# Kernel tuning notes

Hardware: AMD Instinct MI355X
Metric: run time of the kernel (lower is better)

Reference implementation:

```python
import jax, jax.numpy as jnp
import numpy as np

N_NODES = 50000
N_EDGES = 600000
D_IN = 128
D_OUT = 128

def setup_inputs() -> dict:
    key = jax.random.key(0)
    k1, k2, k3, k4 = jax.random.split(key, 4)
    x = jax.random.normal(k1, (N_NODES, D_IN), dtype=jnp.float32)
    edge_index = jax.random.randint(k2, (2, N_EDGES), 0, N_NODES, dtype=jnp.int64)
    # Linear weights stored as (in, out) so y = x @ W + b; scaled like torch default init
    W1 = jax.random.normal(k3, (2 * D_IN, D_OUT), dtype=jnp.float32) * (1.0 / np.sqrt(2 * D_IN))
    b1 = jnp.zeros((D_OUT,), dtype=jnp.float32)
    W2 = jax.random.normal(k4, (D_OUT, D_OUT), dtype=jnp.float32) * (1.0 / np.sqrt(D_OUT))
    b2 = jnp.zeros((D_OUT,), dtype=jnp.float32)
    return {"x": x, "edge_index": edge_index, "W1": W1, "b1": b1, "W2": W2, "b2": b2}

def reference(x, edge_index, W1, b1, W2, b2):
    row, col = edge_index[0], edge_index[1]
    x_col = x[col]                       # [E, D_IN]
    feat = jnp.concatenate([x_col, x[row] - x_col], axis=-1)  # [E, 2*D_IN]
    h = jax.nn.relu(feat @ W1 + b1)      # [E, D_OUT]
    messages = h @ W2 + b2               # [E, D_OUT]
    # max aggregation into nodes, empty segments -> -inf -> 0
    out = jax.ops.segment_max(messages, col, num_segments=x.shape[0])
    out = jnp.where(jnp.isneginf(out), jnp.zeros_like(out), out)
    return out
```

## Files before the change

### kernel.cpp

```cpp
#include <hip/hip_runtime.h>

typedef __attribute__((ext_vector_type(8))) _Float16 f16x8;
typedef __attribute__((ext_vector_type(4))) _Float16 f16x4;
typedef __attribute__((ext_vector_type(4))) float f32x4;

#define D 128
#define NCH 256
#define BNODES 16
#define TILE 64
#define SC_ILP 4
#define PSTRIDE 136

static __device__ __forceinline__ ushort f2h(float f) {
    _Float16 h = (_Float16)f;
    return __builtin_bit_cast(ushort, h);
}

__global__ void prep_kernel(const float* __restrict__ W1,
                            const float* __restrict__ W2,
                            const int* __restrict__ ecol,
                            ushort* __restrict__ w1abt,
                            ushort* __restrict__ w2t,
                            int* __restrict__ hist,
                            int* __restrict__ rank,
                            int E, int n_nodes)
{
    int gid = blockIdx.x * blockDim.x + threadIdx.x;
    if (gid < NCH * D) {
        int oc = gid >> 7, k = gid & 127;
        float v;
        if (oc < 128) v = W1[k * D + oc] - W1[(k + 128) * D + oc];
        else          v = W1[(k + 128) * D + (oc - 128)];
        w1abt[gid] = f2h(v);
    } else if (gid < NCH * D + D * D) {
        int id2 = gid - NCH * D;
        int oc = id2 >> 7, k = id2 & 127;
        w2t[id2] = f2h(W2[k * D + oc]);
    } else {
        int e = gid - (NCH * D + D * D);
        if (e < E) {
            int c = ecol[e];
            if ((unsigned)c >= (unsigned)n_nodes) c = 0;
            rank[e] = atomicAdd(&hist[c], 1);
        }
    }
}

__global__ void scan1_kernel(const int* __restrict__ hist, int* __restrict__ partial, int N)
{
    __shared__ int s[256];
    int tid = threadIdx.x;
    int i = blockIdx.x * 256 + tid;
    s[tid] = (i < N) ? hist[i] : 0;
    __syncthreads();
    #pragma unroll
    for (int off = 128; off > 0; off >>= 1) {
        if (tid < off) s[tid] += s[tid + off];
        __syncthreads();
    }
    if (tid == 0) partial[blockIdx.x] = s[0];
}

__global__ void scan23_kernel(const int* __restrict__ hist, const int* __restrict__ partial,
                              int* __restrict__ ofs,
                              int nb, int N, int E)
{
    __shared__ int sp[256];
    __shared__ int s[256];
    int tid = threadIdx.x;

    int pv = (tid < nb) ? partial[tid] : 0;
    sp[tid] = pv;
    __syncthreads();
    #pragma unroll
    for (int off = 1; off < 256; off <<= 1) {
        int t = (tid >= off) ? sp[tid - off] : 0;
        __syncthreads();
        sp[tid] += t;
        __syncthreads();
    }
    const int bofs = (blockIdx.x > 0) ? sp[blockIdx.x - 1] : 0;

    int i = blockIdx.x * 256 + tid;
    int v = (i < N) ? hist[i] : 0;
    s[tid] = v;
    __syncthreads();
    #pragma unroll
    for (int off = 1; off < 256; off <<= 1) {
        int t = (tid >= off) ? s[tid - off] : 0;
        __syncthreads();
        s[tid] += t;
        __syncthreads();
    }
    if (i < N) ofs[i] = bofs + s[tid] - v;
    if (blockIdx.x == 0 && tid == 0) ofs[N] = E;
}

__global__ __launch_bounds__(256) void scatter_pab_kernel(
    const float* __restrict__ x,
    const ushort* __restrict__ w1abt,
    const float* __restrict__ b1,
    ushort* __restrict__ pab,
    const int* __restrict__ erow, const int* __restrict__ ecol,
    const int* __restrict__ nofs,
    const int* __restrict__ rank,
    unsigned* __restrict__ spk,
    int E, int n_nodes, int npab)
{
    __shared__ ushort A[64 * 128];
    const int tid = threadIdx.x;

    if ((int)blockIdx.x >= npab) {
        const int stride = (gridDim.x - npab) * 256;
        const int e0 = ((int)blockIdx.x - npab) * 256 + tid;
        int cc[SC_ILP], rr[SC_ILP], rk[SC_ILP];
        #pragma unroll
        for (int j = 0; j < SC_ILP; ++j) {
            int e = e0 + j * stride;
            if (e < E) {
                int c = ecol[e];
                if ((unsigned)c >= (unsigned)n_nodes) c = 0;
                int r = erow[e];
                if ((unsigned)r >= (unsigned)n_nodes) r = 0;
                cc[j] = c; rr[j] = r; rk[j] = rank[e];
            } else cc[j] = -1;
        }
        int pos[SC_ILP];
        #pragma unroll
        for (int j = 0; j < SC_ILP; ++j)
            if (cc[j] >= 0) pos[j] = nofs[cc[j]] + rk[j];
        #pragma unroll
        for (int j = 0; j < SC_ILP; ++j)
            if (cc[j] >= 0) spk[pos[j]] = (unsigned)cc[j] | ((unsigned)rr[j] << 16);
        return;
    }

    const int base = blockIdx.x * 64;

    #pragma unroll
    for (int it = 0; it < 8; ++it) {
        int idx4 = it * 256 + tid;
        int row = idx4 >> 5;
        int c4  = idx4 & 31;
        int node = base + row;
        float4 vx = make_float4(0.f, 0.f, 0.f, 0.f);
        if (node < n_nodes) vx = ((const float4*)x)[(size_t)node * 32 + c4];
        f16x4 o;
        o[0] = (_Float16)vx.x; o[1] = (_Float16)vx.y;
        o[2] = (_Float16)vx.z; o[3] = (_Float16)vx.w;
        *(f16x4*)((char*)A + row * 256 + ((c4 * 8) ^ ((row & 7) << 4))) = o;
    }
    __syncthreads();

    const int l = tid & 63, w = tid >> 6;
    const int l15 = l & 15, lq = l >> 4;

    f32x4 acc[4][4];
    #pragma unroll
    for (int cf = 0; cf < 4; ++cf)
        #pragma unroll
        for (int rf = 0; rf < 4; ++rf)
            acc[cf][rf] = (f32x4){0.f, 0.f, 0.f, 0.f};

    #pragma unroll
    for (int kk = 0; kk < 4; ++kk) {
        f16x8 a[4], b[4];
        #pragma unroll
        for (int cf = 0; cf < 4; ++cf)
            a[cf] = *(const f16x8*)(w1abt + (w * 64 + cf * 16 + l15) * 128 + kk * 32 + lq * 8);
        #pragma unroll
        for (int rf = 0; rf < 4; ++rf) {
            int row = rf * 16 + l15;
            b[rf] = *(const f16x8*)((const char*)A + row * 256 + ((kk * 64 + lq * 16) ^ ((row & 7) << 4)));
        }
        #pragma unroll
        for (int cf = 0; cf < 4; ++cf)
            #pragma unroll
            for (int rf = 0; rf < 4; ++rf)
                acc[cf][rf] = __builtin_amdgcn_mfma_f32_16x16x32_f16(a[cf], b[rf], acc[cf][rf], 0, 0, 0);
    }

    #pragma unroll
    for (int rf = 0; rf < 4; ++rf) {
        int node = base + rf * 16 + l15;
        if (node < n_nodes) {
            #pragma unroll
            for (int cf = 0; cf < 4; ++cf) {
                int ch = w * 64 + cf * 16 + lq * 4;
                float4 bb = (w < 2) ? *(const float4*)(b1 + ch) : make_float4(0.f, 0.f, 0.f, 0.f);
                f16x4 o;
                o[0] = (_Float16)(acc[cf][rf][0] + bb.x);
                o[1] = (_Float16)(acc[cf][rf][1] + bb.y);
                o[2] = (_Float16)(acc[cf][rf][2] + bb.z);
                o[3] = (_Float16)(acc[cf][rf][3] + bb.w);
                *(f16x4*)(pab + (size_t)node * NCH + ch) = o;
            }
        }
    }
}

__global__ __launch_bounds__(256, 4) void edgeconv_main(
    const ushort* __restrict__ pab,
    const ushort* __restrict__ w2t,
    const unsigned* __restrict__ spk,
    const int* __restrict__ nofs,
    const float* __restrict__ b2,
    float* __restrict__ out,
    int E, int n_nodes)
{
    __shared__ unsigned outbuf[BNODES * D];
    __shared__ ushort Hs[TILE * D];
    __shared__ ushort PaL[BNODES * PSTRIDE];
    __shared__ int colidx[TILE];
    __shared__ int rowidx[TILE];

    const int tid = threadIdx.x;

    const int nwg = gridDim.x, orig = blockIdx.x;
    const int q = nwg >> 3, rr = nwg & 7, xcd = orig & 7;
    const int bucket = (xcd < rr ? xcd * (q + 1) : rr * (q + 1) + (xcd - rr) * q) + (orig >> 3);

    const int base = bucket * BNODES;
    const int nend = min(base + BNODES, n_nodes);
    const int estart = nofs[base];
    const int eend = nofs[nend];

    #pragma unroll
    for (int i = 0; i < 8; ++i) outbuf[tid + i * 256] = 0u;

    const int l = tid & 63, w = tid >> 6;
    const int l15 = l & 15, lq = l >> 4;
    const int cg = tid & 15, esub = tid >> 4;
    const f16x8 zero = {0, 0, 0, 0, 0, 0, 0, 0};
    const unsigned padp = (unsigned)base | ((unsigned)base << 16);

    {
        int node = tid >> 4;
        int ch = (tid & 15) * 8;
        int gn = base + node;
        f16x8 v = zero;
        if (gn < n_nodes) v = *(const f16x8*)(pab + (size_t)gn * NCH + ch);
        *(f16x8*)(PaL + node * PSTRIDE + ch) = v;
    }

    unsigned px = padp;
    if (tid < TILE && estart + tid < eend) px = spk[estart + tid];

    for (int t0 = estart; t0 < eend; t0 += TILE) {
        const int n = min(TILE, eend - t0);
        __syncthreads();
        if (tid < TILE) {
            colidx[tid] = (int)(px & 0xffffu);
            rowidx[tid] = (int)(px >> 16);
            int nt = t0 + TILE + tid;
            px = (nt < eend) ? spk[nt] : padp;
        }
        __syncthreads();

        {
            f16x8 vb[4];
            #pragma unroll
            for (int it = 0; it < 4; ++it) {
                int e = it * 16 + esub;
                int r = rowidx[e];
                vb[it] = *(const f16x8*)(pab + (size_t)r * NCH + 128 + cg * 8);
            }
            #pragma unroll
            for (int it = 0; it < 4; ++it) {
                int e = it * 16 + esub;
                int c = colidx[e] - base;
                f16x8 va = *(const f16x8*)(PaL + c * PSTRIDE + cg * 8);
                f16x8 h = __builtin_elementwise_max(va + vb[it], zero);
                *(f16x8*)((char*)Hs + e * 256 + ((cg * 16) ^ ((e & 7) << 4))) = h;
            }
        }
        __syncthreads();

        f32x4 acc[4][2];
        #pragma unroll
        for (int mf = 0; mf < 4; ++mf)
            #pragma unroll
            for (int nf = 0; nf < 2; ++nf)
                acc[mf][nf] = (f32x4){0.f, 0.f, 0.f, 0.f};

        #pragma unroll
        for (int kk = 0; kk < 4; ++kk) {
            f16x8 a[4], b[2];
            #pragma unroll
            for (int mf = 0; mf < 4; ++mf) {
                int row = mf * 16 + l15;
                a[mf] = *(const f16x8*)((const char*)Hs + row * 256 + ((kk * 64 + lq * 16) ^ ((row & 7) << 4)));
            }
            #pragma unroll
            for (int nf = 0; nf < 2; ++nf) {
                int col = w * 32 + nf * 16 + l15;
                b[nf] = *(const f16x8*)(w2t + col * 128 + kk * 32 + lq * 8);
            }
            #pragma unroll
            for (int mf = 0; mf < 4; ++mf)
                #pragma unroll
                for (int nf = 0; nf < 2; ++nf)
                    acc[mf][nf] = __builtin_amdgcn_mfma_f32_16x16x32_f16(a[mf], b[nf], acc[mf][nf], 0, 0, 0);
        }

        #pragma unroll
        for (int nf = 0; nf < 2; ++nf) {
            int col = w * 32 + nf * 16 + l15;
            #pragma unroll
            for (int mf = 0; mf < 4; ++mf) {
                #pragma unroll
                for (int r = 0; r < 4; ++r) {
                    int row = mf * 16 + lq * 4 + r;
                    if (row < n) {
                        int node = colidx[row] - base;
                        unsigned bs = __float_as_uint(acc[mf][nf][r]);
                        unsigned enc = (bs & 0x80000000u) ? ~bs : (bs | 0x80000000u);
                        atomicMax(&outbuf[node * D + col], enc);
                    }
                }
            }
        }
    }
    __syncthreads();

    const int n0 = tid >> 4;
    const int c0 = (tid & 15) * 8;
    const int gnode = base + n0;
    if (gnode < n_nodes) {
        #pragma unroll
        for (int j = 0; j < 2; ++j) {
            float4 o;
            #pragma unroll
            for (int k = 0; k < 4; ++k) {
                int ch = c0 + j * 4 + k;
                unsigned u = outbuf[n0 * D + ch];
                float v;
                if (u == 0u) v = 0.f;
                else {
                    unsigned bs = (u & 0x80000000u) ? (u & 0x7fffffffu) : ~u;
                    v = __uint_as_float(bs) + b2[ch];
                }
                ((float*)&o)[k] = v;
            }
            *(float4*)(out + (size_t)gnode * D + c0 + j * 4) = o;
        }
    }
}

extern "C" void kernel_launch(void* const* d_in, const int* in_sizes, int n_in,
                              void* d_out, int out_size, void* d_ws, size_t ws_size,
                              hipStream_t stream)
{
    const float* x  = (const float*)d_in[0];
    const int* eidx = (const int*)d_in[1];
    const float* W1 = (const float*)d_in[2];
    const float* b1 = (const float*)d_in[3];
    const float* W2 = (const float*)d_in[4];
    const float* b2 = (const float*)d_in[5];

    const int n_nodes = in_sizes[0] / D;
    const int E = in_sizes[1] / 2;
    const int* erow = eidx;
    const int* ecol = eidx + E;

    const int nb_scan = (n_nodes + 255) / 256;
    const int nbuckets = (n_nodes + BNODES - 1) / BNODES;
    const int npab = (n_nodes + 63) / 64;
    const int nsc = (E + 256 * SC_ILP - 1) / (256 * SC_ILP);

    char* ws = (char*)d_ws;
    size_t off = 0;
    ushort* pab = (ushort*)(ws + off);   off += (size_t)n_nodes * NCH * sizeof(ushort);
    off = (off + 255) & ~(size_t)255;
    ushort* w1abt = (ushort*)(ws + off); off += (size_t)NCH * D * sizeof(ushort);
    ushort* w2t = (ushort*)(ws + off);   off += (size_t)D * D * sizeof(ushort);
    off = (off + 255) & ~(size_t)255;
    int* hist = (int*)(ws + off);        off += (size_t)n_nodes * 4;
    off = (off + 255) & ~(size_t)255;
    int* nofs = (int*)(ws + off);        off += (size_t)(n_nodes + 1) * 4;
    off = (off + 255) & ~(size_t)255;
    int* rank = (int*)(ws + off);        off += (size_t)E * 4;
    off = (off + 255) & ~(size_t)255;
    int* partial = (int*)(ws + off);     off += 256 * 4;
    off = (off + 255) & ~(size_t)255;
    unsigned* spk = (unsigned*)(ws + off); off += (size_t)E * 4;

    float* out = (float*)d_out;

    hipMemsetAsync(hist, 0, (size_t)n_nodes * sizeof(int), stream);

    const int prep_work = NCH * D + D * D + E;
    prep_kernel<<<(prep_work + 255) / 256, 256, 0, stream>>>(W1, W2, ecol, w1abt, w2t, hist, rank, E, n_nodes);

    scan1_kernel<<<nb_scan, 256, 0, stream>>>(hist, partial, n_nodes);
    scan23_kernel<<<nb_scan, 256, 0, stream>>>(hist, partial, nofs, nb_scan, n_nodes, E);

    scatter_pab_kernel<<<npab + nsc, 256, 0, stream>>>(x, w1abt, b1, pab, erow, ecol,
                                                       nofs, rank, spk, E, n_nodes, npab);

    edgeconv_main<<<nbuckets, 256, 0, stream>>>(pab, w2t, spk, nofs, b2, out, E, n_nodes);
}
```

Baseline: 130.4 us.

## Double-buffer edge indices and prefetch next tile's row gathers during MFMA

Edge column/row indices are now double-buffered in shared memory, and the global gather of the next tile's row features (vb) is issued before the MFMA and atomic-max phase of the current tile. This hides gather latency behind compute and cuts one barrier per tile. The cost is more live registers for the prefetched vectors, which could reduce occupancy, and a more complex sync ordering.

```diff
diff --git a/kernel.cpp b/kernel.cpp
--- a/kernel.cpp
+++ b/kernel.cpp
@@ -211,8 +211,8 @@
     __shared__ unsigned outbuf[BNODES * D];
     __shared__ ushort Hs[TILE * D];
     __shared__ ushort PaL[BNODES * PSTRIDE];
-    __shared__ int colidx[TILE];
-    __shared__ int rowidx[TILE];
+    __shared__ int colb[2][TILE];
+    __shared__ int rowb[2][TILE];
 
     const int tid = threadIdx.x;
 
@@ -245,36 +245,52 @@
 
     unsigned px = padp;
     if (tid < TILE && estart + tid < eend) px = spk[estart + tid];
-
-    for (int t0 = estart; t0 < eend; t0 += TILE) {
+    if (tid < TILE) {
+        colb[0][tid] = (int)(px & 0xffffu);
+        rowb[0][tid] = (int)(px >> 16);
+        int nt1 = estart + TILE + tid;
+        px = (nt1 < eend) ? spk[nt1] : padp;
+    }
+    __syncthreads();
+
+    f16x8 vb[4];
+    if (estart < eend) {
+        #pragma unroll
+        for (int it = 0; it < 4; ++it) {
+            int r = rowb[0][it * 16 + esub];
+            vb[it] = *(const f16x8*)(pab + (size_t)r * NCH + 128 + cg * 8);
+        }
+    }
+
+    int t = 0;
+    for (int t0 = estart; t0 < eend; t0 += TILE, ++t) {
+        const int cur = t & 1, nxt = cur ^ 1;
         const int n = min(TILE, eend - t0);
-        __syncthreads();
+        const bool more = (t0 + TILE) < eend;
+
+        #pragma unroll
+        for (int it = 0; it < 4; ++it) {
+            int e = it * 16 + esub;
+            int c = colb[cur][e] - base;
+            f16x8 va = *(const f16x8*)(PaL + c * PSTRIDE + cg * 8);
+            f16x8 h = __builtin_elementwise_max(va + vb[it], zero);
+            *(f16x8*)((char*)Hs + e * 256 + ((cg * 16) ^ ((e & 7) << 4))) = h;
+        }
         if (tid < TILE) {
-            colidx[tid] = (int)(px & 0xffffu);
-            rowidx[tid] = (int)(px >> 16);
-            int nt = t0 + TILE + tid;
-            px = (nt < eend) ? spk[nt] : padp;
-        }
-        __syncthreads();
-
-        {
-            f16x8 vb[4];
+            colb[nxt][tid] = (int)(px & 0xffffu);
+            rowb[nxt][tid] = (int)(px >> 16);
+            int nn = t0 + 2 * TILE + tid;
+            px = (nn < eend) ? spk[nn] : padp;
+        }
+        __syncthreads();
+
+        if (more) {
             #pragma unroll
             for (int it = 0; it < 4; ++it) {
-                int e = it * 16 + esub;
-                int r = rowidx[e];
+                int r = rowb[nxt][it * 16 + esub];
                 vb[it] = *(const f16x8*)(pab + (size_t)r * NCH + 128 + cg * 8);
             }
-            #pragma unroll
-            for (int it = 0; it < 4; ++it) {
-                int e = it * 16 + esub;
-                int c = colidx[e] - base;
-                f16x8 va = *(const f16x8*)(PaL + c * PSTRIDE + cg * 8);
-                f16x8 h = __builtin_elementwise_max(va + vb[it], zero);
-                *(f16x8*)((char*)Hs + e * 256 + ((cg * 16) ^ ((e & 7) << 4))) = h;
-            }
-        }
-        __syncthreads();
+        }
 
         f32x4 acc[4][2];
         #pragma unroll
@@ -312,7 +328,7 @@
                 for (int r = 0; r < 4; ++r) {
                     int row = mf * 16 + lq * 4 + r;
                     if (row < n) {
-                        int node = colidx[row] - base;
+                        int node = colb[cur][row] - base;
                         unsigned bs = __float_as_uint(acc[mf][nf][r]);
                         unsigned enc = (bs & 0x80000000u) ? ~bs : (bs | 0x80000000u);
                         atomicMax(&outbuf[node * D + col], enc);
@@ -320,8 +336,8 @@
                 }
             }
         }
-    }
-    __syncthreads();
+        __syncthreads();
+    }
 
     const int n0 = tid >> 4;
     const int c0 = (tid & 15) * 8;
```

New measurement: 133.7 us. 1.03x slower.
